# Kernel tuning notes

Hardware: AMD Instinct MI355X
Metric: run time of the kernel (lower is better)

Reference implementation:

```python
import jax, jax.numpy as jnp
import numpy as np

N, E = 100000, 1600000
IN_C, H, C = 256, 4, 64
NEG_SLOPE = 0.2


def setup_inputs() -> dict:
    key = jax.random.key(0)
    k1, k2, k3, k4, k5 = jax.random.split(key, 5)
    x = jax.random.normal(k1, (N, IN_C), dtype=jnp.float32)
    edge_index = jax.random.randint(k2, (2, E), 0, N, dtype=jnp.int64)
    # GATConv params: lin weight [IN_C, H*C], attention vectors [H, C], bias [C] (concat=False)
    W = jax.random.normal(k3, (IN_C, H * C), dtype=jnp.float32) / np.sqrt(IN_C)
    att_src = jax.random.normal(k4, (H, C), dtype=jnp.float32) / np.sqrt(C)
    att_dst = jax.random.normal(k5, (H, C), dtype=jnp.float32) / np.sqrt(C)
    bias = jnp.zeros((C,), dtype=jnp.float32)
    return {"x": x, "edge_index": edge_index, "W": W,
            "att_src": att_src, "att_dst": att_dst, "bias": bias}


def reference(x, edge_index, W, att_src, att_dst, bias):
    n = x.shape[0]
    # GATConv adds self-loops by default
    loops = jnp.arange(n, dtype=edge_index.dtype)
    src = jnp.concatenate([edge_index[0], loops])  # message source j
    dst = jnp.concatenate([edge_index[1], loops])  # message target i

    h = (x @ W).reshape(n, H, C)                       # [N,H,C]
    a_src = jnp.einsum('nhc,hc->nh', h, att_src)       # [N,H]
    a_dst = jnp.einsum('nhc,hc->nh', h, att_dst)       # [N,H]

    e = jax.nn.leaky_relu(a_src[src] + a_dst[dst], NEG_SLOPE)  # [E+N,H]
    m = jax.ops.segment_max(e, dst, num_segments=n)            # per-target max
    e = jnp.exp(e - m[dst])
    denom = jax.ops.segment_sum(e, dst, num_segments=n)
    alpha = e / (denom[dst] + 1e-16)                           # softmax over incoming edges

    out = jax.ops.segment_sum(alpha[:, :, None] * h[src], dst, num_segments=n)  # [N,H,C]
    return out.mean(axis=1) + bias  # concat=False -> mean over heads, [N,C]
```

## Files before the change

### kernel.cpp

```cpp
#include <hip/hip_runtime.h>

#define N_NODES 100000
#define N_EDGES 1600000
#define TOT (N_EDGES + N_NODES)
#define IN_CH 256
#define NHEAD 4
#define CH 64
#define HC 256
#define NEG_SLOPE 0.2f
#define NGEMM ((N_NODES + 63) / 64)
#define DEG_BLOCKS 391

typedef _Float16 half8 __attribute__((ext_vector_type(8)));
typedef _Float16 h2v __attribute__((ext_vector_type(2)));
typedef float f32x4 __attribute__((ext_vector_type(4)));
typedef unsigned short ushort_t;
typedef unsigned int uint_t;

static __device__ __forceinline__ ushort_t f2h(float f) {
  _Float16 h = (_Float16)f;
  return __builtin_bit_cast(ushort_t, h);
}

static __device__ __forceinline__ void gload_lds16(const char* g, char* l) {
  __builtin_amdgcn_global_load_lds(
      (const __attribute__((address_space(1))) unsigned int*)g,
      (__attribute__((address_space(3))) unsigned int*)l, 16, 0, 0);
}

__global__ __launch_bounds__(256) void conv_w(const float* __restrict__ W,
                                              uint4* __restrict__ Wt_arr) {
  int id = blockIdx.x * 256 + threadIdx.x;
  int lane = id & 63;
  int n = (id >> 6) & 15;
  int ks = id >> 10;
  int col = n * 16 + (lane & 15);
  int kbase = ks * 32 + (lane >> 4) * 8;
  ushort_t h[8];
#pragma unroll
  for (int j = 0; j < 8; ++j) h[j] = f2h(W[(size_t)(kbase + j) * HC + col]);
  uint4 u;
  u.x = (uint_t)h[0] | ((uint_t)h[1] << 16);
  u.y = (uint_t)h[2] | ((uint_t)h[3] << 16);
  u.z = (uint_t)h[4] | ((uint_t)h[5] << 16);
  u.w = (uint_t)h[6] | ((uint_t)h[7] << 16);
  Wt_arr[id] = u;
}

__global__ __launch_bounds__(256) void gemm_mfma(const float* __restrict__ X,
                                                 const uint4* __restrict__ Wt_arr,
                                                 const float* __restrict__ att_src,
                                                 const float* __restrict__ att_dst,
                                                 uint2* __restrict__ Hmp,
                                                 float* __restrict__ as_out,
                                                 float* __restrict__ ad_out,
                                                 const int* __restrict__ edst,
                                                 int* __restrict__ deg, int M) {
  const int tid = threadIdx.x;

  if (blockIdx.x >= NGEMM) {
    int db = blockIdx.x - NGEMM;
#pragma unroll
    for (int i = 0; i < 4; ++i) {
      int t = (db * 4 + i) * 256 + tid;
      if (t < N_EDGES / 4) {
        int4 d4 = reinterpret_cast<const int4*>(edst)[t];
        atomicAdd(&deg[d4.x], 1);
        atomicAdd(&deg[d4.y], 1);
        atomicAdd(&deg[d4.z], 1);
        atomicAdd(&deg[d4.w], 1);
      }
    }
    return;
  }

  __shared__ uint4 Bs[3][1024];
  __shared__ __align__(16) float As[3][2048];
  const int lane = tid & 63;
  const int wid = tid >> 6;
  const int l16 = lane & 15;
  const int lhi = lane >> 4;
  const int row0 = blockIdx.x * 64;

  const int arow = tid >> 3;
  const int aslot = tid & 7;
  int ga0 = row0 + arow;       if (ga0 >= M) ga0 = M - 1;
  int ga1 = row0 + arow + 32;  if (ga1 >= M) ga1 = M - 1;
  const int sslot = aslot ^ (arow & 7);
  const char* asrc0 = (const char*)X + (size_t)ga0 * 1024 + (sslot << 4);
  const char* asrc1 = (const char*)X + (size_t)ga1 * 1024 + (sslot << 4);

  const char* __restrict__ wsrc = (const char*)Wt_arr;

  const int frow = wid * 16 + l16;
  const int sw = frow & 7;
  const int fo0 = frow * 32 + (((2 * lhi + 0) ^ sw) << 2);
  const int fo1 = frow * 32 + (((2 * lhi + 1) ^ sw) << 2);

  auto ISSUE = [&](int kk, int b) {
    char* ad = (char*)&As[b][0] + tid * 16;
    gload_lds16(asrc0 + kk * 128, ad);
    gload_lds16(asrc1 + kk * 128, ad + 4096);
    char* bd = (char*)&Bs[b][0] + tid * 16;
    const char* s = wsrc + kk * 16384 + tid * 16;
    gload_lds16(s,         bd);
    gload_lds16(s + 4096,  bd + 4096);
    gload_lds16(s + 8192,  bd + 8192);
    gload_lds16(s + 12288, bd + 12288);
  };

  ISSUE(0, 0);
  ISSUE(1, 1);

  f32x4 acc[16] = {};

#pragma unroll
  for (int ks = 0; ks < 8; ++ks) {
    __builtin_amdgcn_s_barrier();
    if (ks < 6) ISSUE(ks + 2, (ks + 2) % 3);
    if (ks < 6)       asm volatile("s_waitcnt vmcnt(12)" ::: "memory");
    else if (ks == 6) asm volatile("s_waitcnt vmcnt(6)" ::: "memory");
    else              asm volatile("s_waitcnt vmcnt(0)" ::: "memory");

    const float* Ab = &As[ks % 3][0];
    float4 f0 = *reinterpret_cast<const float4*>(Ab + fo0);
    float4 f1 = *reinterpret_cast<const float4*>(Ab + fo1);
    uint4 ua;
    ua.x = __builtin_bit_cast(uint_t, __builtin_amdgcn_cvt_pkrtz(f0.x, f0.y));
    ua.y = __builtin_bit_cast(uint_t, __builtin_amdgcn_cvt_pkrtz(f0.z, f0.w));
    ua.z = __builtin_bit_cast(uint_t, __builtin_amdgcn_cvt_pkrtz(f1.x, f1.y));
    ua.w = __builtin_bit_cast(uint_t, __builtin_amdgcn_cvt_pkrtz(f1.z, f1.w));
    half8 a = __builtin_bit_cast(half8, ua);

    const char* bbase = (const char*)&Bs[ks % 3][0];
#pragma unroll
    for (int n = 0; n < 16; ++n) {
      half8 b = *reinterpret_cast<const half8*>(bbase + n * 1024 + lane * 16);
      acc[n] = __builtin_amdgcn_mfma_f32_16x16x32_f16(a, b, acc[n], 0, 0, 0);
    }
  }

  float attS[16], attD[16];
#pragma unroll
  for (int n = 0; n < 16; ++n) {
    attS[n] = att_src[n * 16 + l16];
    attD[n] = att_dst[n * 16 + l16];
  }

#pragma unroll
  for (int r = 0; r < 4; ++r) {
    int grow = row0 + wid * 16 + lhi * 4 + r;
    if (grow < M) {
#pragma unroll
      for (int n2 = 0; n2 < 4; ++n2) {
        uint_t pk01 = __builtin_bit_cast(uint_t,
            __builtin_amdgcn_cvt_pkrtz(acc[n2][r], acc[n2 + 4][r]));
        uint_t pk23 = __builtin_bit_cast(uint_t,
            __builtin_amdgcn_cvt_pkrtz(acc[n2 + 8][r], acc[n2 + 12][r]));
        Hmp[(size_t)grow * 64 + n2 * 16 + l16] = make_uint2(pk01, pk23);
      }
      float sv[4] = {0.f, 0.f, 0.f, 0.f}, dv[4] = {0.f, 0.f, 0.f, 0.f};
#pragma unroll
      for (int h = 0; h < 4; ++h)
#pragma unroll
        for (int j = 0; j < 4; ++j) {
          sv[h] += acc[h * 4 + j][r] * attS[h * 4 + j];
          dv[h] += acc[h * 4 + j][r] * attD[h * 4 + j];
        }
#pragma unroll
      for (int off = 1; off < 16; off <<= 1)
#pragma unroll
        for (int h = 0; h < 4; ++h) {
          sv[h] += __shfl_xor(sv[h], off, 16);
          dv[h] += __shfl_xor(dv[h], off, 16);
        }
      if (l16 == 0) {
#pragma unroll
        for (int h = 0; h < 4; ++h) {
          as_out[(size_t)grow * 4 + h] = sv[h];
          ad_out[(size_t)grow * 4 + h] = dv[h];
        }
      }
    }
  }
}

__global__ __launch_bounds__(256) void scan1(const int* __restrict__ deg,
                                             int* __restrict__ rp,
                                             int* __restrict__ bsum) {
  __shared__ int sh[256];
  int t = threadIdx.x;
  int base = blockIdx.x * 1024 + t * 4;
  int v[4];
#pragma unroll
  for (int i = 0; i < 4; ++i) v[i] = (base + i < N_NODES) ? (deg[base + i] + 1) : 0;
  int tsum = v[0] + v[1] + v[2] + v[3];
  sh[t] = tsum;
  __syncthreads();
  for (int off = 1; off < 256; off <<= 1) {
    int x = (t >= off) ? sh[t - off] : 0;
    __syncthreads();
    sh[t] += x;
    __syncthreads();
  }
  if (t == 255) bsum[blockIdx.x] = sh[255];
  int run = sh[t] - tsum;
#pragma unroll
  for (int i = 0; i < 4; ++i) {
    if (base + i < N_NODES) rp[base + i] = run;
    run += v[i];
  }
}

#define NBLK1 ((N_NODES + 1023) / 1024)

__global__ __launch_bounds__(128) void scan2(const int* __restrict__ bsum,
                                             int* __restrict__ boff) {
  __shared__ int sh[128];
  int t = threadIdx.x;
  int own = (t < NBLK1) ? bsum[t] : 0;
  sh[t] = own;
  __syncthreads();
  for (int off = 1; off < 128; off <<= 1) {
    int x = (t >= off) ? sh[t - off] : 0;
    __syncthreads();
    sh[t] += x;
    __syncthreads();
  }
  boff[t] = sh[t] - own;
}

__global__ __launch_bounds__(256) void scan3(int* __restrict__ rp,
                                             const int* __restrict__ boff,
                                             int* __restrict__ cursor) {
  int idx = blockIdx.x * 256 + threadIdx.x;
  if (idx < N_NODES) {
    int v = rp[idx] + boff[idx >> 10];
    rp[idx] = v;
    cursor[idx] = v;
  }
  if (idx == 0) rp[N_NODES] = TOT;
}

__global__ __launch_bounds__(256) void scatter_edges(const int* __restrict__ esrc,
                                                     const int* __restrict__ edst,
                                                     const float* __restrict__ as_buf,
                                                     const float* __restrict__ ad_buf,
                                                     int* __restrict__ cursor,
                                                     uint4* __restrict__ erec) {
  int e = blockIdx.x * 256 + threadIdx.x;
  if (e >= TOT) return;
  int s, d;
  if (e < N_EDGES) { s = esrc[e]; d = edst[e]; }
  else { s = e - N_EDGES; d = s; }
  int p = atomicAdd(&cursor[d], 1);
  float4 a1 = *reinterpret_cast<const float4*>(as_buf + (size_t)s * NHEAD);
  float4 a2 = *reinterpret_cast<const float4*>(ad_buf + (size_t)d * NHEAD);
  float e0 = a1.x + a2.x; e0 = e0 > 0.f ? e0 : NEG_SLOPE * e0;
  float e1 = a1.y + a2.y; e1 = e1 > 0.f ? e1 : NEG_SLOPE * e1;
  float e2 = a1.z + a2.z; e2 = e2 > 0.f ? e2 : NEG_SLOPE * e2;
  float e3 = a1.w + a2.w; e3 = e3 > 0.f ? e3 : NEG_SLOPE * e3;
  float w0 = __expf(e0 - 4.f), w1 = __expf(e1 - 4.f);
  float w2 = __expf(e2 - 4.f), w3 = __expf(e3 - 4.f);
  uint_t pk01 = __builtin_bit_cast(uint_t, __builtin_amdgcn_cvt_pkrtz(w0, w1));
  uint_t pk23 = __builtin_bit_cast(uint_t, __builtin_amdgcn_cvt_pkrtz(w2, w3));
  erec[p] = make_uint4((uint_t)s, pk01, pk23, 0u);
}

static __device__ __forceinline__ void accum_edge(uint4 cur, uint4 hv, bool act,
                                                  float* acc, float* den) {
  uint_t w01u = act ? cur.y : 0u;
  uint_t w23u = act ? cur.z : 0u;
  h2v w01 = __builtin_bit_cast(h2v, w01u);
  h2v w23 = __builtin_bit_cast(h2v, w23u);
  h2v ha = __builtin_bit_cast(h2v, hv.x);
  h2v hb = __builtin_bit_cast(h2v, hv.y);
  h2v hc = __builtin_bit_cast(h2v, hv.z);
  h2v hd = __builtin_bit_cast(h2v, hv.w);
  acc[0] += (float)w01.x * (float)ha.x;
  acc[1] += (float)w01.y * (float)ha.y;
  acc[2] += (float)w23.x * (float)hb.x;
  acc[3] += (float)w23.y * (float)hb.y;
  acc[4] += (float)w01.x * (float)hc.x;
  acc[5] += (float)w01.y * (float)hc.y;
  acc[6] += (float)w23.x * (float)hd.x;
  acc[7] += (float)w23.y * (float)hd.y;
  den[0] += (float)w01.x;
  den[1] += (float)w01.y;
  den[2] += (float)w23.x;
  den[3] += (float)w23.y;
}

__global__ __launch_bounds__(256) void aggregate(const int* __restrict__ rp,
                                                 const uint4* __restrict__ erec,
                                                 const uint2* __restrict__ Hp,
                                                 const float* __restrict__ bias,
                                                 float* __restrict__ out) {
  int n = blockIdx.x * 4 + (threadIdx.x >> 6);
  int lane = threadIdx.x & 63;
  if (n >= N_NODES) return;
  const int half = lane >> 5;
  const uint_t off_lane = (uint_t)(lane & 31) << 4;
  const char* __restrict__ Hb = (const char*)Hp;

  int beg = rp[n], end = rp[n + 1];

  float acc[8] = {};
  float den[4] = {};

  int j = beg;
  if (j + 15 < end) {
    const uint4* ep = erec + j + half;
    uint4 r0 = ep[0], r1 = ep[2], r2 = ep[4], r3 = ep[6];
    for (; j + 15 < end; j += 8, ep += 8) {
      uint4 c0 = r0, c1 = r1, c2 = r2, c3 = r3;
      r0 = ep[8]; r1 = ep[10]; r2 = ep[12]; r3 = ep[14];
      uint4 h0 = *reinterpret_cast<const uint4*>(Hb + ((c0.x << 9) | off_lane));
      uint4 h1 = *reinterpret_cast<const uint4*>(Hb + ((c1.x << 9) | off_lane));
      uint4 h2 = *reinterpret_cast<const uint4*>(Hb + ((c2.x << 9) | off_lane));
      uint4 h3 = *reinterpret_cast<const uint4*>(Hb + ((c3.x << 9) | off_lane));
      accum_edge(c0, h0, true, acc, den);
      accum_edge(c1, h1, true, acc, den);
      accum_edge(c2, h2, true, acc, den);
      accum_edge(c3, h3, true, acc, den);
    }
  }
  if (j < end) {
    const int last = end - 1;
    int i0 = j + half;     if (i0 > last) i0 = last;
    int i1 = j + 2 + half; if (i1 > last) i1 = last;
    int i2 = j + 4 + half; if (i2 > last) i2 = last;
    int i3 = j + 6 + half; if (i3 > last) i3 = last;
    uint4 r0 = erec[i0], r1 = erec[i1], r2 = erec[i2], r3 = erec[i3];
    for (; j < end; j += 8) {
      uint4 c0 = r0, c1 = r1, c2 = r2, c3 = r3;
      i0 = j + 8 + half;  if (i0 > last) i0 = last;
      i1 = j + 10 + half; if (i1 > last) i1 = last;
      i2 = j + 12 + half; if (i2 > last) i2 = last;
      i3 = j + 14 + half; if (i3 > last) i3 = last;
      r0 = erec[i0]; r1 = erec[i1]; r2 = erec[i2]; r3 = erec[i3];
      uint4 h0 = *reinterpret_cast<const uint4*>(Hb + ((c0.x << 9) | off_lane));
      uint4 h1 = *reinterpret_cast<const uint4*>(Hb + ((c1.x << 9) | off_lane));
      uint4 h2 = *reinterpret_cast<const uint4*>(Hb + ((c2.x << 9) | off_lane));
      uint4 h3 = *reinterpret_cast<const uint4*>(Hb + ((c3.x << 9) | off_lane));
      accum_edge(c0, h0, (j + half) < end, acc, den);
      accum_edge(c1, h1, (j + 2 + half) < end, acc, den);
      accum_edge(c2, h2, (j + 4 + half) < end, acc, den);
      accum_edge(c3, h3, (j + 6 + half) < end, acc, den);
    }
  }

#pragma unroll
  for (int k = 0; k < 8; ++k) acc[k] += __shfl_xor(acc[k], 32, 64);
#pragma unroll
  for (int k = 0; k < 4; ++k) den[k] += __shfl_xor(den[k], 32, 64);

  if (lane < 32) {
    float i0v = 1.f / (den[0] + 1e-30f);
    float i1v = 1.f / (den[1] + 1e-30f);
    float i2v = 1.f / (den[2] + 1e-30f);
    float i3v = 1.f / (den[3] + 1e-30f);
    float2 b2 = *reinterpret_cast<const float2*>(bias + 2 * lane);
    float rA = 0.25f * (acc[0] * i0v + acc[1] * i1v + acc[2] * i2v + acc[3] * i3v) + b2.x;
    float rB = 0.25f * (acc[4] * i0v + acc[5] * i1v + acc[6] * i2v + acc[7] * i3v) + b2.y;
    *reinterpret_cast<float2*>(out + (size_t)n * CH + 2 * lane) = make_float2(rA, rB);
  }
}

extern "C" void kernel_launch(void* const* d_in, const int* in_sizes, int n_in,
                              void* d_out, int out_size, void* d_ws, size_t ws_size,
                              hipStream_t stream) {
  const float* x       = (const float*)d_in[0];
  const int*   eidx    = (const int*)d_in[1];
  const float* W       = (const float*)d_in[2];
  const float* att_src = (const float*)d_in[3];
  const float* att_dst = (const float*)d_in[4];
  const float* bias    = (const float*)d_in[5];
  float* out = (float*)d_out;

  uint2* Hmp    = (uint2*)d_ws;
  uint4* erec   = (uint4*)(Hmp + (size_t)N_NODES * 64);
  float* as_buf = (float*)(erec + (size_t)TOT + 16);
  float* ad_buf = as_buf + (size_t)N_NODES * NHEAD;
  uint4* Wt_arr = (uint4*)(ad_buf + (size_t)N_NODES * NHEAD);
  int*   deg    = (int*)(Wt_arr + 8192);
  int*   rp     = deg + N_NODES;
  int*   bsum   = rp + N_NODES + 1;
  int*   boff   = bsum + 128;

  const int* esrc = eidx;
  const int* edst = eidx + N_EDGES;

  conv_w<<<32, 256, 0, stream>>>(W, Wt_arr);
  hipMemsetAsync(deg, 0, (size_t)N_NODES * sizeof(int), stream);

  dim3 ggrid(NGEMM + DEG_BLOCKS);
  gemm_mfma<<<ggrid, 256, 0, stream>>>(x, Wt_arr, att_src, att_dst, Hmp, as_buf, ad_buf,
                                       edst, deg, N_NODES);

  scan1<<<NBLK1, 256, 0, stream>>>(deg, rp, bsum);
  scan2<<<1, 128, 0, stream>>>(bsum, boff);
  scan3<<<(N_NODES + 255) / 256, 256, 0, stream>>>(rp, boff, deg );
  scatter_edges<<<(TOT + 255) / 256, 256, 0, stream>>>(esrc, edst, as_buf, ad_buf,
                                                       deg , erec);

  aggregate<<<(N_NODES + 3) / 4, 256, 0, stream>>>(rp, erec, Hmp, bias, out);
}
```

Measured before the change: 316.5 us.

## Reorder degree blocks first, pair edges in scatter, simplify aggregate tail

Degree-count blocks now take the low block indices of the fused GEMM launch, so the edge atomics are dispatched before the GEMM tiles. The scatter kernel handles two edges per thread with vectorized int2 index loads. The aggregate main loop now runs whenever at least 8 edges remain, and its prefetch can read past the node's edge range. To keep those reads safe, a 16-record zeroed pad is written after the edge records, and the remainder loop becomes a single masked pass. The aim is fewer tail iterations and less per-thread launch overhead, at the cost of extra prefetch reads past each node's edges.

```diff
diff --git a/kernel.cpp b/kernel.cpp
--- a/kernel.cpp
+++ b/kernel.cpp
@@ -58,11 +58,10 @@
                                                  int* __restrict__ deg, int M) {
   const int tid = threadIdx.x;
 
-  if (blockIdx.x >= NGEMM) {
-    int db = blockIdx.x - NGEMM;
+  if (blockIdx.x < DEG_BLOCKS) {
 #pragma unroll
     for (int i = 0; i < 4; ++i) {
-      int t = (db * 4 + i) * 256 + tid;
+      int t = (blockIdx.x * 4 + i) * 256 + tid;
       if (t < N_EDGES / 4) {
         int4 d4 = reinterpret_cast<const int4*>(edst)[t];
         atomicAdd(&deg[d4.x], 1);
@@ -80,7 +79,7 @@
   const int wid = tid >> 6;
   const int l16 = lane & 15;
   const int lhi = lane >> 4;
-  const int row0 = blockIdx.x * 64;
+  const int row0 = (blockIdx.x - DEG_BLOCKS) * 64;
 
   const int arow = tid >> 3;
   const int aslot = tid & 7;
@@ -242,17 +241,11 @@
   if (idx == 0) rp[N_NODES] = TOT;
 }
 
-__global__ __launch_bounds__(256) void scatter_edges(const int* __restrict__ esrc,
-                                                     const int* __restrict__ edst,
-                                                     const float* __restrict__ as_buf,
-                                                     const float* __restrict__ ad_buf,
-                                                     int* __restrict__ cursor,
-                                                     uint4* __restrict__ erec) {
-  int e = blockIdx.x * 256 + threadIdx.x;
-  if (e >= TOT) return;
-  int s, d;
-  if (e < N_EDGES) { s = esrc[e]; d = edst[e]; }
-  else { s = e - N_EDGES; d = s; }
+static __device__ __forceinline__ void scatter_one(int s, int d,
+                                                   const float* __restrict__ as_buf,
+                                                   const float* __restrict__ ad_buf,
+                                                   int* __restrict__ cursor,
+                                                   uint4* __restrict__ erec) {
   int p = atomicAdd(&cursor[d], 1);
   float4 a1 = *reinterpret_cast<const float4*>(as_buf + (size_t)s * NHEAD);
   float4 a2 = *reinterpret_cast<const float4*>(ad_buf + (size_t)d * NHEAD);
@@ -265,6 +258,33 @@
   uint_t pk01 = __builtin_bit_cast(uint_t, __builtin_amdgcn_cvt_pkrtz(w0, w1));
   uint_t pk23 = __builtin_bit_cast(uint_t, __builtin_amdgcn_cvt_pkrtz(w2, w3));
   erec[p] = make_uint4((uint_t)s, pk01, pk23, 0u);
+}
+
+__global__ __launch_bounds__(256) void scatter_edges(const int* __restrict__ esrc,
+                                                     const int* __restrict__ edst,
+                                                     const float* __restrict__ as_buf,
+                                                     const float* __restrict__ ad_buf,
+                                                     int* __restrict__ cursor,
+                                                     uint4* __restrict__ erec) {
+  int g = blockIdx.x * 256 + threadIdx.x;
+  int e0 = 2 * g;
+  if (e0 >= TOT) return;
+  if (e0 + 1 < N_EDGES) {
+    int2 s2 = *reinterpret_cast<const int2*>(esrc + e0);
+    int2 d2 = *reinterpret_cast<const int2*>(edst + e0);
+    scatter_one(s2.x, d2.x, as_buf, ad_buf, cursor, erec);
+    scatter_one(s2.y, d2.y, as_buf, ad_buf, cursor, erec);
+  } else {
+#pragma unroll
+    for (int i = 0; i < 2; ++i) {
+      int e = e0 + i;
+      if (e >= TOT) break;
+      int s, d;
+      if (e < N_EDGES) { s = esrc[e]; d = edst[e]; }
+      else { s = e - N_EDGES; d = s; }
+      scatter_one(s, d, as_buf, ad_buf, cursor, erec);
+    }
+  }
 }
 
 static __device__ __forceinline__ void accum_edge(uint4 cur, uint4 hv, bool act,
@@ -309,10 +329,10 @@
   float den[4] = {};
 
   int j = beg;
-  if (j + 15 < end) {
+  if (j + 7 < end) {
     const uint4* ep = erec + j + half;
     uint4 r0 = ep[0], r1 = ep[2], r2 = ep[4], r3 = ep[6];
-    for (; j + 15 < end; j += 8, ep += 8) {
+    for (; j + 7 < end; j += 8, ep += 8) {
       uint4 c0 = r0, c1 = r1, c2 = r2, c3 = r3;
       r0 = ep[8]; r1 = ep[10]; r2 = ep[12]; r3 = ep[14];
       uint4 h0 = *reinterpret_cast<const uint4*>(Hb + ((c0.x << 9) | off_lane));
@@ -331,23 +351,15 @@
     int i1 = j + 2 + half; if (i1 > last) i1 = last;
     int i2 = j + 4 + half; if (i2 > last) i2 = last;
     int i3 = j + 6 + half; if (i3 > last) i3 = last;
-    uint4 r0 = erec[i0], r1 = erec[i1], r2 = erec[i2], r3 = erec[i3];
-    for (; j < end; j += 8) {
-      uint4 c0 = r0, c1 = r1, c2 = r2, c3 = r3;
-      i0 = j + 8 + half;  if (i0 > last) i0 = last;
-      i1 = j + 10 + half; if (i1 > last) i1 = last;
-      i2 = j + 12 + half; if (i2 > last) i2 = last;
-      i3 = j + 14 + half; if (i3 > last) i3 = last;
-      r0 = erec[i0]; r1 = erec[i1]; r2 = erec[i2]; r3 = erec[i3];
-      uint4 h0 = *reinterpret_cast<const uint4*>(Hb + ((c0.x << 9) | off_lane));
-      uint4 h1 = *reinterpret_cast<const uint4*>(Hb + ((c1.x << 9) | off_lane));
-      uint4 h2 = *reinterpret_cast<const uint4*>(Hb + ((c2.x << 9) | off_lane));
-      uint4 h3 = *reinterpret_cast<const uint4*>(Hb + ((c3.x << 9) | off_lane));
-      accum_edge(c0, h0, (j + half) < end, acc, den);
-      accum_edge(c1, h1, (j + 2 + half) < end, acc, den);
-      accum_edge(c2, h2, (j + 4 + half) < end, acc, den);
-      accum_edge(c3, h3, (j + 6 + half) < end, acc, den);
-    }
+    uint4 c0 = erec[i0], c1 = erec[i1], c2 = erec[i2], c3 = erec[i3];
+    uint4 h0 = *reinterpret_cast<const uint4*>(Hb + ((c0.x << 9) | off_lane));
+    uint4 h1 = *reinterpret_cast<const uint4*>(Hb + ((c1.x << 9) | off_lane));
+    uint4 h2 = *reinterpret_cast<const uint4*>(Hb + ((c2.x << 9) | off_lane));
+    uint4 h3 = *reinterpret_cast<const uint4*>(Hb + ((c3.x << 9) | off_lane));
+    accum_edge(c0, h0, (j + half) < end, acc, den);
+    accum_edge(c1, h1, (j + 2 + half) < end, acc, den);
+    accum_edge(c2, h2, (j + 4 + half) < end, acc, den);
+    accum_edge(c3, h3, (j + 6 + half) < end, acc, den);
   }
 
 #pragma unroll
@@ -393,16 +405,18 @@
 
   conv_w<<<32, 256, 0, stream>>>(W, Wt_arr);
   hipMemsetAsync(deg, 0, (size_t)N_NODES * sizeof(int), stream);
-
-  dim3 ggrid(NGEMM + DEG_BLOCKS);
+  hipMemsetAsync(erec + (size_t)TOT, 0, 16 * sizeof(uint4), stream);
+
+  dim3 ggrid(DEG_BLOCKS + NGEMM);
   gemm_mfma<<<ggrid, 256, 0, stream>>>(x, Wt_arr, att_src, att_dst, Hmp, as_buf, ad_buf,
                                        edst, deg, N_NODES);
 
   scan1<<<NBLK1, 256, 0, stream>>>(deg, rp, bsum);
   scan2<<<1, 128, 0, stream>>>(bsum, boff);
   scan3<<<(N_NODES + 255) / 256, 256, 0, stream>>>(rp, boff, deg );
-  scatter_edges<<<(TOT + 255) / 256, 256, 0, stream>>>(esrc, edst, as_buf, ad_buf,
-                                                       deg , erec);
+  scatter_edges<<<((TOT + 1) / 2 + 255) / 256, 256, 0, stream>>>(esrc, edst, as_buf,
+                                                                 ad_buf, deg ,
+                                                                 erec);
 
   aggregate<<<(N_NODES + 3) / 4, 256, 0, stream>>>(rp, erec, Hmp, bias, out);
 }
```

New measurement: 316.2 us. Within noise of the previous version (-0.1%).

## Use fma_mix fp16 accumulation, relax main-loop bound, reorder fused degree blocks

Applied to the files above, without the earlier changes.

Replaces per-element fp16-to-fp32 conversions plus FMAs in aggregation with v_fma_mix_f32 inline asm operating directly on packed halves, including the denominator sums. Relaxes the unrolled loop bound so more edges go through the fast path, making the tail a single non-looping pass, and zero-pads the edge record array so over-reads stay in bounds. Also places degree-counting blocks first in the fused GEMM grid so atomics start earlier. Inline asm may limit compiler scheduling.

```diff
diff --git a/kernel.cpp b/kernel.cpp
--- a/kernel.cpp
+++ b/kernel.cpp
@@ -12,7 +12,6 @@
 #define DEG_BLOCKS 391
 
 typedef _Float16 half8 __attribute__((ext_vector_type(8)));
-typedef _Float16 h2v __attribute__((ext_vector_type(2)));
 typedef float f32x4 __attribute__((ext_vector_type(4)));
 typedef unsigned short ushort_t;
 typedef unsigned int uint_t;
@@ -58,11 +57,10 @@
                                                  int* __restrict__ deg, int M) {
   const int tid = threadIdx.x;
 
-  if (blockIdx.x >= NGEMM) {
-    int db = blockIdx.x - NGEMM;
+  if (blockIdx.x < DEG_BLOCKS) {
 #pragma unroll
     for (int i = 0; i < 4; ++i) {
-      int t = (db * 4 + i) * 256 + tid;
+      int t = (blockIdx.x * 4 + i) * 256 + tid;
       if (t < N_EDGES / 4) {
         int4 d4 = reinterpret_cast<const int4*>(edst)[t];
         atomicAdd(&deg[d4.x], 1);
@@ -80,7 +78,7 @@
   const int wid = tid >> 6;
   const int l16 = lane & 15;
   const int lhi = lane >> 4;
-  const int row0 = blockIdx.x * 64;
+  const int row0 = (blockIdx.x - DEG_BLOCKS) * 64;
 
   const int arow = tid >> 3;
   const int aslot = tid & 7;
@@ -267,28 +265,32 @@
   erec[p] = make_uint4((uint_t)s, pk01, pk23, 0u);
 }
 
-static __device__ __forceinline__ void accum_edge(uint4 cur, uint4 hv, bool act,
-                                                  float* acc, float* den) {
-  uint_t w01u = act ? cur.y : 0u;
-  uint_t w23u = act ? cur.z : 0u;
-  h2v w01 = __builtin_bit_cast(h2v, w01u);
-  h2v w23 = __builtin_bit_cast(h2v, w23u);
-  h2v ha = __builtin_bit_cast(h2v, hv.x);
-  h2v hb = __builtin_bit_cast(h2v, hv.y);
-  h2v hc = __builtin_bit_cast(h2v, hv.z);
-  h2v hd = __builtin_bit_cast(h2v, hv.w);
-  acc[0] += (float)w01.x * (float)ha.x;
-  acc[1] += (float)w01.y * (float)ha.y;
-  acc[2] += (float)w23.x * (float)hb.x;
-  acc[3] += (float)w23.y * (float)hb.y;
-  acc[4] += (float)w01.x * (float)hc.x;
-  acc[5] += (float)w01.y * (float)hc.y;
-  acc[6] += (float)w23.x * (float)hd.x;
-  acc[7] += (float)w23.y * (float)hd.y;
-  den[0] += (float)w01.x;
-  den[1] += (float)w01.y;
-  den[2] += (float)w23.x;
-  den[3] += (float)w23.y;
+static __device__ __forceinline__ void accum_mix(uint_t w01u, uint_t w23u, uint4 hv,
+                                                 float* acc, float* den, float one) {
+  asm("v_fma_mix_f32 %0, %1, %2, %0 op_sel:[0,0,0] op_sel_hi:[1,1,0]"
+      : "+v"(acc[0]) : "v"(w01u), "v"(hv.x));
+  asm("v_fma_mix_f32 %0, %1, %2, %0 op_sel:[1,1,0] op_sel_hi:[1,1,0]"
+      : "+v"(acc[1]) : "v"(w01u), "v"(hv.x));
+  asm("v_fma_mix_f32 %0, %1, %2, %0 op_sel:[0,0,0] op_sel_hi:[1,1,0]"
+      : "+v"(acc[2]) : "v"(w23u), "v"(hv.y));
+  asm("v_fma_mix_f32 %0, %1, %2, %0 op_sel:[1,1,0] op_sel_hi:[1,1,0]"
+      : "+v"(acc[3]) : "v"(w23u), "v"(hv.y));
+  asm("v_fma_mix_f32 %0, %1, %2, %0 op_sel:[0,0,0] op_sel_hi:[1,1,0]"
+      : "+v"(acc[4]) : "v"(w01u), "v"(hv.z));
+  asm("v_fma_mix_f32 %0, %1, %2, %0 op_sel:[1,1,0] op_sel_hi:[1,1,0]"
+      : "+v"(acc[5]) : "v"(w01u), "v"(hv.z));
+  asm("v_fma_mix_f32 %0, %1, %2, %0 op_sel:[0,0,0] op_sel_hi:[1,1,0]"
+      : "+v"(acc[6]) : "v"(w23u), "v"(hv.w));
+  asm("v_fma_mix_f32 %0, %1, %2, %0 op_sel:[1,1,0] op_sel_hi:[1,1,0]"
+      : "+v"(acc[7]) : "v"(w23u), "v"(hv.w));
+  asm("v_fma_mix_f32 %0, %1, %2, %0 op_sel:[0,0,0] op_sel_hi:[1,0,0]"
+      : "+v"(den[0]) : "v"(w01u), "v"(one));
+  asm("v_fma_mix_f32 %0, %1, %2, %0 op_sel:[1,0,0] op_sel_hi:[1,0,0]"
+      : "+v"(den[1]) : "v"(w01u), "v"(one));
+  asm("v_fma_mix_f32 %0, %1, %2, %0 op_sel:[0,0,0] op_sel_hi:[1,0,0]"
+      : "+v"(den[2]) : "v"(w23u), "v"(one));
+  asm("v_fma_mix_f32 %0, %1, %2, %0 op_sel:[1,0,0] op_sel_hi:[1,0,0]"
+      : "+v"(den[3]) : "v"(w23u), "v"(one));
 }
 
 __global__ __launch_bounds__(256) void aggregate(const int* __restrict__ rp,
@@ -302,6 +304,7 @@
   const int half = lane >> 5;
   const uint_t off_lane = (uint_t)(lane & 31) << 4;
   const char* __restrict__ Hb = (const char*)Hp;
+  const float one = 1.0f;
 
   int beg = rp[n], end = rp[n + 1];
 
@@ -309,20 +312,20 @@
   float den[4] = {};
 
   int j = beg;
-  if (j + 15 < end) {
+  if (j + 7 < end) {
     const uint4* ep = erec + j + half;
     uint4 r0 = ep[0], r1 = ep[2], r2 = ep[4], r3 = ep[6];
-    for (; j + 15 < end; j += 8, ep += 8) {
+    for (; j + 7 < end; j += 8, ep += 8) {
       uint4 c0 = r0, c1 = r1, c2 = r2, c3 = r3;
       r0 = ep[8]; r1 = ep[10]; r2 = ep[12]; r3 = ep[14];
       uint4 h0 = *reinterpret_cast<const uint4*>(Hb + ((c0.x << 9) | off_lane));
       uint4 h1 = *reinterpret_cast<const uint4*>(Hb + ((c1.x << 9) | off_lane));
       uint4 h2 = *reinterpret_cast<const uint4*>(Hb + ((c2.x << 9) | off_lane));
       uint4 h3 = *reinterpret_cast<const uint4*>(Hb + ((c3.x << 9) | off_lane));
-      accum_edge(c0, h0, true, acc, den);
-      accum_edge(c1, h1, true, acc, den);
-      accum_edge(c2, h2, true, acc, den);
-      accum_edge(c3, h3, true, acc, den);
+      accum_mix(c0.y, c0.z, h0, acc, den, one);
+      accum_mix(c1.y, c1.z, h1, acc, den, one);
+      accum_mix(c2.y, c2.z, h2, acc, den, one);
+      accum_mix(c3.y, c3.z, h3, acc, den, one);
     }
   }
   if (j < end) {
@@ -331,23 +334,20 @@
     int i1 = j + 2 + half; if (i1 > last) i1 = last;
     int i2 = j + 4 + half; if (i2 > last) i2 = last;
     int i3 = j + 6 + half; if (i3 > last) i3 = last;
-    uint4 r0 = erec[i0], r1 = erec[i1], r2 = erec[i2], r3 = erec[i3];
-    for (; j < end; j += 8) {
-      uint4 c0 = r0, c1 = r1, c2 = r2, c3 = r3;
-      i0 = j + 8 + half;  if (i0 > last) i0 = last;
-      i1 = j + 10 + half; if (i1 > last) i1 = last;
-      i2 = j + 12 + half; if (i2 > last) i2 = last;
-      i3 = j + 14 + half; if (i3 > last) i3 = last;
-      r0 = erec[i0]; r1 = erec[i1]; r2 = erec[i2]; r3 = erec[i3];
-      uint4 h0 = *reinterpret_cast<const uint4*>(Hb + ((c0.x << 9) | off_lane));
-      uint4 h1 = *reinterpret_cast<const uint4*>(Hb + ((c1.x << 9) | off_lane));
-      uint4 h2 = *reinterpret_cast<const uint4*>(Hb + ((c2.x << 9) | off_lane));
-      uint4 h3 = *reinterpret_cast<const uint4*>(Hb + ((c3.x << 9) | off_lane));
-      accum_edge(c0, h0, (j + half) < end, acc, den);
-      accum_edge(c1, h1, (j + 2 + half) < end, acc, den);
-      accum_edge(c2, h2, (j + 4 + half) < end, acc, den);
-      accum_edge(c3, h3, (j + 6 + half) < end, acc, den);
-    }
+    uint4 c0 = erec[i0], c1 = erec[i1], c2 = erec[i2], c3 = erec[i3];
+    uint4 h0 = *reinterpret_cast<const uint4*>(Hb + ((c0.x << 9) | off_lane));
+    uint4 h1 = *reinterpret_cast<const uint4*>(Hb + ((c1.x << 9) | off_lane));
+    uint4 h2 = *reinterpret_cast<const uint4*>(Hb + ((c2.x << 9) | off_lane));
+    uint4 h3 = *reinterpret_cast<const uint4*>(Hb + ((c3.x << 9) | off_lane));
+    uint_t w01, w23;
+    w01 = (j + half) < end ? c0.y : 0u;     w23 = (j + half) < end ? c0.z : 0u;
+    accum_mix(w01, w23, h0, acc, den, one);
+    w01 = (j + 2 + half) < end ? c1.y : 0u; w23 = (j + 2 + half) < end ? c1.z : 0u;
+    accum_mix(w01, w23, h1, acc, den, one);
+    w01 = (j + 4 + half) < end ? c2.y : 0u; w23 = (j + 4 + half) < end ? c2.z : 0u;
+    accum_mix(w01, w23, h2, acc, den, one);
+    w01 = (j + 6 + half) < end ? c3.y : 0u; w23 = (j + 6 + half) < end ? c3.z : 0u;
+    accum_mix(w01, w23, h3, acc, den, one);
   }
 
 #pragma unroll
@@ -393,8 +393,9 @@
 
   conv_w<<<32, 256, 0, stream>>>(W, Wt_arr);
   hipMemsetAsync(deg, 0, (size_t)N_NODES * sizeof(int), stream);
-
-  dim3 ggrid(NGEMM + DEG_BLOCKS);
+  hipMemsetAsync(erec + (size_t)TOT, 0, 16 * sizeof(uint4), stream);
+
+  dim3 ggrid(DEG_BLOCKS + NGEMM);
   gemm_mfma<<<ggrid, 256, 0, stream>>>(x, Wt_arr, att_src, att_dst, Hmp, as_buf, ad_buf,
                                        edst, deg, N_NODES);
 
```

New measurement: 314.5 us. Within noise of the previous version (-0.6%).
